# Kernel optimization log

Hardware: AMD Instinct MI355X
Metric: run time of the kernel (lower is better)

Reference implementation:

```python
import jax, jax.numpy as jnp
import numpy as np

B, L, N = 8, 720, 321
D_MODEL, H, E_LAYERS, PRED = 512, 8, 2, 336
D_HEAD = D_MODEL // H
D_FF = 128
FACTOR = 5
U = min(int(FACTOR * np.ceil(np.log(L))), L)  # = 35: top-u queries and sample size
EPS = 1e-5


def _layer_norm(x, g, b):
    mu = x.mean(-1, keepdims=True)
    var = ((x - mu) ** 2).mean(-1, keepdims=True)
    return (x - mu) / jnp.sqrt(var + EPS) * g + b


def _prob_attention(q, k, v, samp_idx):
    # Informer ProbSparse attention (mask_flag=False). q,k,v: [B,H,L,Dh]
    Bq, Hq, Lq, Dh = q.shape
    k_samp = k[:, :, samp_idx, :]                                   # [B,H,L,S,Dh]
    qk_samp = jnp.einsum('bhld,bhlsd->bhls', q, k_samp)             # sampled scores
    M = qk_samp.max(-1) - qk_samp.sum(-1) / Lq                      # sparsity measure
    _, m_top = jax.lax.top_k(M, U)                                  # [B,H,U]
    q_red = jnp.take_along_axis(q, m_top[..., None], axis=2)        # [B,H,U,Dh]
    scores = jnp.einsum('bhud,bhld->bhul', q_red, k) * (1.0 / np.sqrt(Dh))
    attn = jax.nn.softmax(scores, axis=-1)
    upd = jnp.einsum('bhul,bhld->bhud', attn, v)                    # [B,H,U,Dh]
    ctx = jnp.broadcast_to(v.mean(axis=2, keepdims=True), q.shape)  # mean-V init
    b_idx = jnp.arange(Bq)[:, None, None]
    h_idx = jnp.arange(Hq)[None, :, None]
    return ctx.at[b_idx, h_idx, m_top].set(upd)


def _forward(x_enc, embed_w, embed_b, wq, bq, wk, bk, wv, bv, wo, bo,
             ln1_g, ln1_b, w1, b1, w2, b2, ln2_g, ln2_b,
             wout, bout, wg, bg, samp_idx):
    x = jnp.transpose(x_enc, (0, 2, 1))                             # [B,N,L]
    mean = x.mean(-1, keepdims=True)
    std = jnp.std(x, axis=-1, ddof=1, keepdims=True) + EPS
    xs = (x - mean) / std
    h = jnp.transpose(xs, (0, 2, 1)) @ embed_w + embed_b            # [B,L,Dm]
    y = jnp.zeros((B, L, PRED), dtype=h.dtype)

    def heads(t):
        return jnp.transpose(t.reshape(B, L, H, D_HEAD), (0, 2, 1, 3))

    for l in range(E_LAYERS):
        q = heads(h @ wq[l] + bq[l])
        k = heads(h @ wk[l] + bk[l])
        v = heads(h @ wv[l] + bv[l])
        ctx = _prob_attention(q, k, v, samp_idx)
        ctx = jnp.transpose(ctx, (0, 2, 1, 3)).reshape(B, L, D_MODEL)
        attn_out = ctx @ wo[l] + bo[l]
        hx = _layer_norm(h - attn_out, ln1_g[l], ln1_b[l])          # Minusformer subtraction
        ff = jax.nn.relu(hx @ w1[l] + b1[l]) @ w2[l] + b2[l]
        h = _layer_norm(hx - ff, ln2_g[l], ln2_b[l])
        y = y + (h @ wout[l] + bout[l]) * jax.nn.sigmoid(h @ wg[l] + bg[l])
    out = y[:, :N, :] * std + mean                                  # inverse scaling [B,N,PRED]
    return jnp.transpose(out, (0, 2, 1))                            # [B,PRED,N]


def setup_inputs() -> dict:
    key = jax.random.key(0)
    ks = jax.random.split(key, 12)
    s = 0.02

    def w(k, shape):
        return jax.random.normal(k, shape, dtype=jnp.float32) * s

    return {
        'x_enc': jax.random.normal(ks[0], (B, L, N), dtype=jnp.float32),
        'samp_idx': jax.random.randint(ks[1], (L, U), 0, L),
        'embed_w': w(ks[2], (N, D_MODEL)),
        'embed_b': jnp.zeros((D_MODEL,), jnp.float32),
        'wq': w(ks[3], (E_LAYERS, D_MODEL, D_MODEL)),
        'bq': jnp.zeros((E_LAYERS, D_MODEL), jnp.float32),
        'wk': w(ks[4], (E_LAYERS, D_MODEL, D_MODEL)),
        'bk': jnp.zeros((E_LAYERS, D_MODEL), jnp.float32),
        'wv': w(ks[5], (E_LAYERS, D_MODEL, D_MODEL)),
        'bv': jnp.zeros((E_LAYERS, D_MODEL), jnp.float32),
        'wo': w(ks[6], (E_LAYERS, D_MODEL, D_MODEL)),
        'bo': jnp.zeros((E_LAYERS, D_MODEL), jnp.float32),
        'ln1_g': jnp.ones((E_LAYERS, D_MODEL), jnp.float32),
        'ln1_b': jnp.zeros((E_LAYERS, D_MODEL), jnp.float32),
        'w1': w(ks[7], (E_LAYERS, D_MODEL, D_FF)),
        'b1': jnp.zeros((E_LAYERS, D_FF), jnp.float32),
        'w2': w(ks[8], (E_LAYERS, D_FF, D_MODEL)),
        'b2': jnp.zeros((E_LAYERS, D_MODEL), jnp.float32),
        'ln2_g': jnp.ones((E_LAYERS, D_MODEL), jnp.float32),
        'ln2_b': jnp.zeros((E_LAYERS, D_MODEL), jnp.float32),
        'wout': w(ks[9], (E_LAYERS, D_MODEL, PRED)),
        'bout': jnp.zeros((E_LAYERS, PRED), jnp.float32),
        'wg': w(ks[10], (E_LAYERS, D_MODEL, PRED)),
        'bg': jnp.zeros((E_LAYERS, PRED), jnp.float32),
    }


def reference(x_enc, samp_idx, embed_w, embed_b, wq, bq, wk, bk, wv, bv, wo, bo,
              ln1_g, ln1_b, w1, b1, w2, b2, ln2_g, ln2_b, wout, bout, wg, bg):
    return _forward(x_enc, embed_w, embed_b, wq, bq, wk, bk, wv, bv, wo, bo,
                    ln1_g, ln1_b, w1, b1, w2, b2, ln2_g, ln2_b,
                    wout, bout, wg, bg, samp_idx)
```

## Files before the change

kernel.cpp:

```cpp
#include <hip/hip_runtime.h>
#include <math.h>

#define BB_ 8
#define LL_ 720
#define NF 321
#define DM 512
#define HH_ 8
#define DH 64
#define DFF 128
#define PRED 336
#define UK 35
#define NLAY 2
#define EPSF 1e-5f
#define BL (BB_*LL_)
#define TJC 72
#define NCH (LL_/TJC)
#define LCH 48
#define NLC (LL_/LCH)

typedef unsigned short ushort;
typedef __attribute__((ext_vector_type(4))) float f32x4;
typedef __attribute__((ext_vector_type(8))) ushort ushort8;
typedef __attribute__((ext_vector_type(4))) ushort ushortx4;

#define KVSEG ((size_t)64*LL_*64)

__device__ __forceinline__ float b2f(ushort u){
  unsigned int x = ((unsigned int)u) << 16;
  return __builtin_bit_cast(float, x);
}
__device__ __forceinline__ ushort f2b(float f){
  unsigned int x = __builtin_bit_cast(unsigned int, f);
  unsigned int r = x + 0x7fff + ((x >> 16) & 1);
  return (ushort)(r >> 16);
}

__device__ __forceinline__ float wredsum(float v){
#pragma unroll
  for (int o=32;o>0;o>>=1) v += __shfl_xor(v,o,64);
  return v;
}
__device__ __forceinline__ float wredmax(float v){
#pragma unroll
  for (int o=32;o>0;o>>=1) v = fmaxf(v,__shfl_xor(v,o,64));
  return v;
}
__device__ __forceinline__ float bredsum(float v, float* red){
  int lane = threadIdx.x & 63, wid = threadIdx.x >> 6;
  v = wredsum(v);
  __syncthreads();
  if (lane==0) red[wid]=v;
  __syncthreads();
  return red[0]+red[1]+red[2]+red[3];
}

__global__ __launch_bounds__(256) void stats3_k(const float* __restrict__ x,
                                                float* __restrict__ pp){
  __shared__ float s1[4][64], s2[4][64];
  int blk = blockIdx.x;
  int lc = blk % NLC; int r = blk / NLC;
  int nt = r % 6; int b = r / 6;
  int nl = threadIdx.x & 63, lg = threadIdx.x >> 6;
  int n = nt*64 + nl;
  float sum=0.f, ss=0.f;
  if (n < NF){
    const float* xp = x + ((size_t)b*LL_ + lc*LCH)*NF + n;
    for (int l=lg; l<LCH; l+=4){ float v = xp[(size_t)l*NF]; sum += v; ss = fmaf(v,v,ss); }
  }
  s1[lg][nl]=sum; s2[lg][nl]=ss;
  __syncthreads();
  if (lg==0){
    float S = s1[0][nl]+s1[1][nl]+s1[2][nl]+s1[3][nl];
    float Q = s2[0][nl]+s2[1][nl]+s2[2][nl]+s2[3][nl];
    pp[(size_t)blk*128 + nl]      = S;
    pp[(size_t)blk*128 + 64 + nl] = Q;
  }
}

__global__ __launch_bounds__(64) void statsc_k(const float* __restrict__ pp,
                                               float* __restrict__ mean,
                                               float* __restrict__ stdv,
                                               float* __restrict__ rstd){
  int bn6 = blockIdx.x;
  int nl = threadIdx.x;
  int nt = bn6 % 6, b = bn6 / 6;
  int n = nt*64 + nl;
  if (n >= NF) return;
  float S=0.f, Q=0.f;
#pragma unroll
  for (int lc=0; lc<NLC; ++lc){
    size_t base = ((size_t)(b*6+nt)*NLC + lc)*128;
    S += pp[base + nl];
    Q += pp[base + 64 + nl];
  }
  float mu = S*(1.f/LL_);
  float var = fmaxf((Q - S*mu)*(1.f/(LL_-1)), 0.f);
  float sd = sqrtf(var) + EPSF;
  int bn = b*NF+n;
  mean[bn]=mu; stdv[bn]=sd; rstd[bn]=1.f/sd;
}

#define KPE 352
__global__ __launch_bounds__(256) void xnorm_k(const float* __restrict__ x,
                                               const float* __restrict__ mean,
                                               const float* __restrict__ rstd,
                                               ushort* __restrict__ xn){
  int idx = blockIdx.x*256 + threadIdx.x;
  if (idx >= BL*KPE) return;
  int c = idx % KPE; int bl = idx / KPE; int b = bl / LL_;
  float v = 0.f;
  if (c < NF) v = (x[(size_t)bl*NF + c] - mean[b*NF+c]) * rstd[b*NF+c];
  xn[idx] = f2b(v);
}

struct TDesc { const float* in; ushort* out; int N, K, Npad, Kpad, nbx, blk0, ilv; };
struct TPack { TDesc d[17]; int n; };
__global__ __launch_bounds__(256) void transpose_k(TPack p){
  __shared__ float tile[32][33];
  int blk = blockIdx.x;
  int di = 0;
  while (di+1 < p.n && p.d[di+1].blk0 <= blk) ++di;
  TDesc D = p.d[di];
  int rel = blk - D.blk0;
  int bx = rel % D.nbx, by = rel / D.nbx;
  int k0 = bx*32, n0 = by*32;
  int t = threadIdx.x; int tx = t & 31, ty = t >> 5;
#pragma unroll
  for (int i=0;i<4;++i){
    int k = k0+ty+8*i, n = n0+tx;
    float v = (k < D.K && n < D.N) ? D.in[(size_t)k*D.N + n] : 0.f;
    tile[ty+8*i][tx] = v;
  }
  __syncthreads();
#pragma unroll
  for (int i=0;i<4;++i){
    int n = n0+ty+8*i, k = k0+tx;
    if (n < D.Npad && k < D.Kpad){
      int outn = D.ilv ? (2*n + (D.ilv-1)) : n;
      D.out[(size_t)outn*D.Kpad + k] = f2b(tile[tx][ty+8*i]);
    }
  }
}

__global__ __launch_bounds__(256) void pack_bias_k(const float* __restrict__ bq,
                                                   const float* __restrict__ bk,
                                                   const float* __restrict__ bv,
                                                   const float* __restrict__ bo2,
                                                   const float* __restrict__ bg,
                                                   float* __restrict__ bqkv,
                                                   float* __restrict__ bog){
  int t = blockIdx.x*256 + threadIdx.x;
  if (t < 2*1536){
    int l = t/1536, c = t%1536;
    float v = c<512 ? bq[l*512+c] : (c<1024 ? bk[l*512+c-512] : bv[l*512+c-1024]);
    bqkv[t] = v;
  }
  if (t < 2*672){
    int l = t/672, c = t%672;
    int p = c>>1;
    bog[t] = (c&1) ? bg[l*336+p] : bo2[l*336+p];
  }
}

__global__ __launch_bounds__(256) void gemm_k(
    const ushort* __restrict__ A, const ushort* __restrict__ Bt,
    const float* __restrict__ bias, void* __restrict__ Cout,
    ushort* __restrict__ Cbf, ushort* __restrict__ kvp,
    int N, int K, int flags)
{
  __shared__ ushort As[128*32];
  __shared__ ushort Bs[128*32];
  const int t = threadIdx.x;
  const int bm = blockIdx.y << 7, bn = blockIdx.x << 7;
  const int lane = t & 63, wid = t >> 6;
  const int wm = (wid >> 1) << 6, wn = (wid & 1) << 6;
  const int fr = lane & 15, kg = lane >> 4;

  f32x4 acc[4][4];
#pragma unroll
  for (int i=0;i<4;++i)
#pragma unroll
    for (int j=0;j<4;++j) acc[i][j] = (f32x4){0.f,0.f,0.f,0.f};

  const int rA0 = t >> 2,        qA0 = t & 3;
  const int rA1 = (t+256) >> 2;
  const size_t aOff0 = (size_t)(bm + rA0)*K + qA0*8;
  const size_t aOff1 = (size_t)(bm + rA1)*K + qA0*8;
  const size_t bOff0 = (size_t)(bn + rA0)*K + qA0*8;
  const size_t bOff1 = (size_t)(bn + rA1)*K + qA0*8;
  const int lA0 = (rA0<<5) + ((qA0 ^ ((rA0>>1)&3))<<3);
  const int lA1 = (rA1<<5) + ((qA0 ^ ((rA1>>1)&3))<<3);

  for (int k0=0; k0<K; k0+=32){
    ushort8 va0 = *(const ushort8*)(A  + aOff0 + k0);
    ushort8 va1 = *(const ushort8*)(A  + aOff1 + k0);
    ushort8 vb0 = *(const ushort8*)(Bt + bOff0 + k0);
    ushort8 vb1 = *(const ushort8*)(Bt + bOff1 + k0);
    *(ushort8*)&As[lA0] = va0;
    *(ushort8*)&As[lA1] = va1;
    *(ushort8*)&Bs[lA0] = vb0;
    *(ushort8*)&Bs[lA1] = vb1;
    __syncthreads();
    ushort8 af[4], bfr[4];
#pragma unroll
    for (int i=0;i<4;++i){
      int ra = wm + (i<<4) + fr;
      af[i]  = *(const ushort8*)&As[(ra<<5) + ((kg ^ ((ra>>1)&3))<<3)];
      int rb = wn + (i<<4) + fr;
      bfr[i] = *(const ushort8*)&Bs[(rb<<5) + ((kg ^ ((rb>>1)&3))<<3)];
    }
#pragma unroll
    for (int i=0;i<4;++i)
#pragma unroll
      for (int j=0;j<4;++j)
        asm("v_mfma_f32_16x16x32_bf16 %0, %1, %2, %0"
            : "+v"(acc[i][j]) : "v"(af[i]), "v"(bfr[j]));
    __syncthreads();
  }

  const int colBase = bn + wn + fr;
  const int rowBase = bm + wm + (kg << 2);

  if (flags & 16){
#pragma unroll
    for (int j=0;j<4;++j){
      int col = colBase + (j<<4);
      if (col >= N) continue;
      float bv = bias[col];
#pragma unroll
      for (int i=0;i<4;++i){
        int row0 = rowBase + (i<<4);
#pragma unroll
        for (int r=0;r<4;++r){
          float v = acc[i][j][r] + bv;
          float o = __shfl_xor(v, 1, 64);
          if ((lane & 1) == 0){
            float val = v * (1.f/(1.f+__expf(-o)));
            size_t yi = (size_t)(row0+r)*PRED + (col>>1);
            float* yp = (float*)Cout;
            yp[yi] = (flags & 32) ? (yp[yi] + val) : val;
          }
        }
      }
    }
    return;
  }

#pragma unroll
  for (int j=0;j<4;++j){
    int col = colBase + (j<<4);
    if (col >= N) continue;
    float bv = bias[col];
#pragma unroll
    for (int i=0;i<4;++i){
      int row0 = rowBase + (i<<4);
#pragma unroll
      for (int r=0;r<4;++r){
        float v = acc[i][j][r] + bv;
        if (flags & 1) v = fmaxf(v, 0.f);
        int row = row0 + r;
        size_t idx = (size_t)row*N + col;
        if (flags & 2) ((ushort*)Cout)[idx] = f2b(v);
        else if (flags & 8){
          if (col < 512) ((float*)Cout)[idx] = v;
          else {
            int hh = (col >> 6) & 7;
            int dd = col & 63;
            int bb = row / LL_; int jr = row - bb*LL_;
            ushort bfv = f2b(v);
            if (col < 1024){
              kvp[((size_t)(bb*8+hh)*64 + dd)*LL_ + jr] = bfv;
              kvp[2*KVSEG + ((size_t)(bb*8+hh)*LL_ + jr)*64 + dd] = bfv;
            } else {
              kvp[KVSEG + ((size_t)(bb*8+hh)*LL_ + jr)*64 + dd] = bfv;
            }
          }
        } else {
          ((float*)Cout)[idx] = v;
          if (flags & 4) Cbf[idx] = f2b(v);
        }
      }
    }
  }
}

__global__ __launch_bounds__(256) void msc_k(const float* __restrict__ qkv,
                                             const ushort* __restrict__ kR,
                                             const int* __restrict__ samp,
                                             float* __restrict__ Mb){
  __shared__ float sq[4][64];
  int wid = threadIdx.x >> 6, lane = threadIdx.x & 63;
  int gid = blockIdx.x*4 + wid;
  int l = gid % LL_; int bh = gid / LL_; int h = bh & 7; int b = bh >> 3;
  sq[wid][lane] = qkv[(size_t)(b*LL_ + l)*1536 + h*64 + lane];
  __syncthreads();
  float acc = 0.f;
  if (lane < UK){
    int j = samp[l*UK + lane];
    const ushort8* kr = (const ushort8*)(kR + ((size_t)bh*LL_ + j)*64);
    const float* sqw = sq[wid];
#pragma unroll
    for (int d8=0; d8<8; ++d8){
      ushort8 kk = kr[d8];
#pragma unroll
      for (int e=0;e<8;++e) acc = fmaf(sqw[d8*8+e], b2f(kk[e]), acc);
    }
  }
  float mx = (lane < UK) ? acc : -INFINITY;
  float sm = (lane < UK) ? acc : 0.f;
  mx = wredmax(mx);
  sm = wredsum(sm);
  if (lane == 0) Mb[gid] = mx - sm*(1.f/LL_);
}

__global__ __launch_bounds__(64) void topk2_k(const float* __restrict__ Mb,
                                              int* __restrict__ mtop){
  int bh = blockIdx.x; int lane = threadIdx.x;
  const float* mp = Mb + (size_t)bh*LL_;
  float v[12]; int vi[12];
#pragma unroll
  for (int i=0;i<12;++i){
    int j = lane + i*64;
    bool ok = j < LL_;
    v[i] = ok ? mp[j] : -INFINITY;
    vi[i] = ok ? j : (LL_ + i);
  }
  for (int it=0; it<UK; ++it){
    float best = v[0]; int bi = vi[0]; int bslot = 0;
#pragma unroll
    for (int i=1;i<12;++i){
      if (v[i] > best || (v[i]==best && vi[i] < bi)){ best=v[i]; bi=vi[i]; bslot=i; }
    }
    float gb = best; int gi = bi;
#pragma unroll
    for (int o=32;o>0;o>>=1){
      float ov = __shfl_xor(gb,o,64); int oi = __shfl_xor(gi,o,64);
      if (ov > gb || (ov==gb && oi < gi)){ gb=ov; gi=oi; }
    }
    if (lane==0) mtop[(size_t)bh*UK + it] = gi;
    if (bi == gi){
#pragma unroll
      for (int i=0;i<12;++i) if (i==bslot) v[i] = -INFINITY;
    }
  }
}

__global__ __launch_bounds__(256) void vmean_k(const ushort* __restrict__ vp,
                                               float* __restrict__ vmn){
  __shared__ float part[4][64];
  int bh = blockIdx.x;
  int t = threadIdx.x; int d = t & 63, jg = t >> 6;
  const ushort* vb = vp + (size_t)bh*LL_*64 + d;
  float s = 0.f;
  for (int j=jg; j<LL_; j+=4) s += b2f(vb[(size_t)j*64]);
  part[jg][d] = s;
  __syncthreads();
  if (t < 64) vmn[bh*64+t] = (part[0][t]+part[1][t]+part[2][t]+part[3][t])*(1.f/LL_);
}

__global__ __launch_bounds__(256) void ctxfill_k(const float* __restrict__ vmn,
                                                 ushort* __restrict__ ctx){
  int idx = blockIdx.x*256 + threadIdx.x;
  int c4 = idx & 127; int bl = idx >> 7; int b = bl / LL_;
  int c = c4*4;
  const float* vm = vmn + (b*8 + (c>>6))*64 + (c&63);
  ushortx4 o = { f2b(vm[0]), f2b(vm[1]), f2b(vm[2]), f2b(vm[3]) };
  *(ushortx4*)&ctx[(size_t)bl*DM + c] = o;
}

__global__ __launch_bounds__(256) void attn4_k(const float* __restrict__ qkv,
                                               const ushort* __restrict__ kT,
                                               const ushort* __restrict__ vp,
                                               const int* __restrict__ mtop,
                                               float* __restrict__ pacc,
                                               float* __restrict__ pm,
                                               float* __restrict__ pl){
  __shared__ ushort skT[64][TJC];
  __shared__ ushort sv[TJC][64];
  __shared__ float  sq[UK][64];
  __shared__ float  sc[UK][TJC];
  int blk = blockIdx.x;
  int ch = blk % NCH; int bh = blk / NCH;
  int b = bh >> 3, h = bh & 7; int t0 = ch*TJC;
  int t = threadIdx.x, lane = t & 63, wid = t >> 6;
  for (int idx=t; idx<64*(TJC/8); idx+=256){
    int d = idx/(TJC/8), c8 = idx%(TJC/8);
    *(ushort8*)&skT[d][c8*8] =
      *(const ushort8*)(kT + ((size_t)bh*64 + d)*LL_ + t0 + c8*8);
  }
  for (int idx=t; idx<TJC*8; idx+=256){
    int jj = idx>>3, c8 = idx&7;
    *(ushort8*)&sv[jj][c8*8] =
      *(const ushort8*)(vp + ((size_t)bh*LL_ + t0+jj)*64 + c8*8);
  }
  for (int idx=t; idx<UK*64; idx+=256){
    int u = idx>>6, d = idx&63;
    int row = mtop[bh*UK + u];
    sq[u][d] = qkv[(size_t)(b*LL_ + row)*1536 + h*64 + d];
  }
  __syncthreads();
  for (int idx=t; idx<UK*(TJC/8); idx+=256){
    int u = idx/(TJC/8), jb = idx%(TJC/8);
    float dot[8] = {0.f,0.f,0.f,0.f,0.f,0.f,0.f,0.f};
    const float* qu = sq[u];
#pragma unroll
    for (int d=0; d<64; ++d){
      ushort8 kk = *(const ushort8*)&skT[d][jb*8];
      float qv = qu[d];
#pragma unroll
      for (int e=0;e<8;++e) dot[e] = fmaf(qv, b2f(kk[e]), dot[e]);
    }
#pragma unroll
    for (int e=0;e<8;++e) sc[u][jb*8+e] = dot[e]*0.125f;
  }
  __syncthreads();
  for (int u=wid; u<UK; u+=4){
    float v0 = sc[u][lane];
    float v1 = (lane < TJC-64) ? sc[u][64+lane] : -3.0e38f;
    float mx = wredmax(fmaxf(v0,v1));
    float e0 = __expf(v0-mx);
    float e1 = (lane < TJC-64) ? __expf(v1-mx) : 0.f;
    sc[u][lane] = e0;
    if (lane < TJC-64) sc[u][64+lane] = e1;
    float s = wredsum(e0+e1);
    if (lane==0){
      pm[((size_t)bh*NCH+ch)*UK + u] = mx;
      pl[((size_t)bh*NCH+ch)*UK + u] = s;
    }
  }
  __syncthreads();
  for (int idx=t; idx<UK*64; idx+=256){
    int u = idx>>6, d = idx&63;
    const float* scu = sc[u];
    float a = 0.f;
#pragma unroll 8
    for (int jj=0; jj<TJC; ++jj) a = fmaf(scu[jj], b2f(sv[jj][d]), a);
    pacc[(((size_t)bh*NCH+ch)*UK + u)*64 + d] = a;
  }
}

__global__ __launch_bounds__(256) void attn5_k(const float* __restrict__ pacc,
                                               const float* __restrict__ pm,
                                               const float* __restrict__ pl,
                                               const int* __restrict__ mtop,
                                               ushort* __restrict__ ctx){
  int bh = blockIdx.x; int b = bh >> 3, h = bh & 7;
  int t = threadIdx.x;
  for (int idx=t; idx<UK*64; idx+=256){
    int u = idx>>6, d = idx&63;
    float M = -3.0e38f;
#pragma unroll
    for (int ch=0; ch<NCH; ++ch)
      M = fmaxf(M, pm[((size_t)bh*NCH+ch)*UK + u]);
    float L = 0.f, A = 0.f;
#pragma unroll
    for (int ch=0; ch<NCH; ++ch){
      float w = __expf(pm[((size_t)bh*NCH+ch)*UK + u] - M);
      L += w * pl[((size_t)bh*NCH+ch)*UK + u];
      A += w * pacc[(((size_t)bh*NCH+ch)*UK + u)*64 + d];
    }
    int row = mtop[bh*UK + u];
    ctx[(size_t)(b*LL_ + row)*DM + h*64 + d] = f2b(A / L);
  }
}

__global__ __launch_bounds__(256) void subln_k(const float* __restrict__ a,
                                               const float* __restrict__ s,
                                               const float* __restrict__ g,
                                               const float* __restrict__ be,
                                               float* __restrict__ of32,
                                               ushort* __restrict__ obf){
  __shared__ float red[4];
  int row = blockIdx.x;
  size_t base = (size_t)row * DM;
  int t = threadIdx.x;
  float e0 = a[base+t]     - s[base+t];
  float e1 = a[base+t+256] - s[base+t+256];
  float sum = bredsum(e0+e1, red);
  float mu = sum * (1.f/DM);
  float d0 = e0-mu, d1 = e1-mu;
  __syncthreads();
  float var = bredsum(d0*d0+d1*d1, red);
  float rs = rsqrtf(var*(1.f/DM) + EPSF);
  float o0 = d0*rs*g[t]     + be[t];
  float o1 = d1*rs*g[t+256] + be[t+256];
  of32[base+t]     = o0;
  of32[base+t+256] = o1;
  obf[base+t]      = f2b(o0);
  obf[base+t+256]  = f2b(o1);
}

__global__ __launch_bounds__(256) void final2_k(const float* __restrict__ y,
                                                const float* __restrict__ stdv,
                                                const float* __restrict__ mean,
                                                float* __restrict__ out){
  __shared__ float tile[32][33];
  int n0 = blockIdx.x*32, p0 = blockIdx.y*32, b = blockIdx.z;
  int tx = threadIdx.x & 31, ty = threadIdx.x >> 5;
  for (int i=ty; i<32; i+=8){
    int n = n0+i, p = p0+tx;
    tile[i][tx] = (n<NF && p<PRED) ? y[((size_t)b*LL_+n)*PRED + p] : 0.f;
  }
  __syncthreads();
  for (int i=ty; i<32; i+=8){
    int p = p0+i, n = n0+tx;
    if (p<PRED && n<NF)
      out[((size_t)b*PRED + p)*NF + n] = tile[tx][i]*stdv[b*NF+n] + mean[b*NF+n];
  }
}

extern "C" void kernel_launch(void* const* d_in, const int* in_sizes, int n_in,
                              void* d_out, int out_size, void* d_ws, size_t ws_size,
                              hipStream_t stream){
  const float* x_enc = (const float*)d_in[0];
  const int*   samp  = (const int*)  d_in[1];
  const float* embw  = (const float*)d_in[2];
  const float* embb  = (const float*)d_in[3];
  const float* wq    = (const float*)d_in[4];
  const float* bq    = (const float*)d_in[5];
  const float* wk    = (const float*)d_in[6];
  const float* bk    = (const float*)d_in[7];
  const float* wv    = (const float*)d_in[8];
  const float* bv    = (const float*)d_in[9];
  const float* wo    = (const float*)d_in[10];
  const float* bo    = (const float*)d_in[11];
  const float* ln1g  = (const float*)d_in[12];
  const float* ln1b  = (const float*)d_in[13];
  const float* w1    = (const float*)d_in[14];
  const float* b1    = (const float*)d_in[15];
  const float* w2    = (const float*)d_in[16];
  const float* b2    = (const float*)d_in[17];
  const float* ln2g  = (const float*)d_in[18];
  const float* ln2b  = (const float*)d_in[19];
  const float* wout  = (const float*)d_in[20];
  const float* boutp = (const float*)d_in[21];
  const float* wg    = (const float*)d_in[22];
  const float* bg    = (const float*)d_in[23];
  float* out = (float*)d_out;

  char* wsb = (char*)d_ws;
  size_t off = 0;
  auto alloc = [&](size_t bytes)->void*{
    void* p = wsb + off; off += (bytes + 255) & ~(size_t)255; return p;
  };
  float* mean  = (float*)alloc((size_t)BB_*NF*4);
  float* stdv  = (float*)alloc((size_t)BB_*NF*4);
  float* rstd  = (float*)alloc((size_t)BB_*NF*4);
  float* pp    = (float*)alloc((size_t)BB_*6*NLC*128*4);
  float* bqkv  = (float*)alloc(2*1536*4);
  float* bog   = (float*)alloc(2*672*4);
  ushort* xn     = (ushort*)alloc((size_t)BL*KPE*2);
  ushort* we_t   = (ushort*)alloc((size_t)512*KPE*2);
  ushort* wqkv_t = (ushort*)alloc((size_t)2*1536*512*2);
  ushort* wo_t   = (ushort*)alloc((size_t)2*512*512*2);
  ushort* w1_t   = (ushort*)alloc((size_t)2*128*512*2);
  ushort* w2_t   = (ushort*)alloc((size_t)2*512*128*2);
  ushort* wog_t  = (ushort*)alloc((size_t)2*768*512*2);
  ushort* h_bf   = (ushort*)alloc((size_t)BL*DM*2);
  ushort* hx_bf  = (ushort*)alloc((size_t)BL*DM*2);
  ushort* ctx_bf = (ushort*)alloc((size_t)BL*DM*2);
  ushort* ff1_bf = (ushort*)alloc((size_t)BL*DFF*2);
  ushort* kvpack = (ushort*)alloc(3*KVSEG*2);
  float* h_f32   = (float*)alloc((size_t)BL*DM*4);
  float* hx_f32  = (float*)alloc((size_t)BL*DM*4);
  float* qkv = (float*)alloc((size_t)BL*1536*4);
  float* tmp = (float*)alloc((size_t)BL*DM*4);
  float* y   = (float*)alloc((size_t)BL*PRED*4);
  float* Mb  = (float*)alloc((size_t)BB_*HH_*LL_*4);
  int*  mtop = (int*)  alloc((size_t)BB_*HH_*UK*4);
  float* vmn = (float*)alloc((size_t)BB_*HH_*DH*4);
  float* pacc = (float*)alloc((size_t)64*NCH*UK*64*4);
  float* pm   = (float*)alloc((size_t)64*NCH*UK*4);
  float* pl   = (float*)alloc((size_t)64*NCH*UK*4);
  if (off > ws_size) return;
  ushort* kTp   = kvpack;
  ushort* vpack = kvpack + KVSEG;
  ushort* kRp   = kvpack + 2*KVSEG;

  stats3_k<<<BB_*6*NLC, 256, 0, stream>>>(x_enc, pp);
  statsc_k<<<BB_*6, 64, 0, stream>>>(pp, mean, stdv, rstd);
  xnorm_k<<<(BL*KPE+255)/256, 256, 0, stream>>>(x_enc, mean, rstd, xn);

  TPack tp; int blk = 0; int di = 0;
  auto addT = [&](const float* in, ushort* o, int N, int K, int Npad, int Kpad, int ilv){
    TDesc& d = tp.d[di++]; d.in=in; d.out=o; d.N=N; d.K=K; d.Npad=Npad; d.Kpad=Kpad; d.ilv=ilv;
    d.nbx = (Kpad+31)/32; d.blk0 = blk; blk += d.nbx * ((Npad+31)/32);
  };
  addT(embw, we_t, 512, NF, 512, KPE, 0);
  for (int l=0;l<NLAY;++l){
    addT(wq + (size_t)l*262144, wqkv_t + (size_t)l*786432,            512,512,512,512,0);
    addT(wk + (size_t)l*262144, wqkv_t + (size_t)l*786432 + 262144,   512,512,512,512,0);
    addT(wv + (size_t)l*262144, wqkv_t + (size_t)l*786432 + 524288,   512,512,512,512,0);
    addT(wo + (size_t)l*262144, wo_t   + (size_t)l*262144,            512,512,512,512,0);
    addT(w1 + (size_t)l*65536,  w1_t   + (size_t)l*65536,             128,512,128,512,0);
    addT(w2 + (size_t)l*65536,  w2_t   + (size_t)l*65536,             512,128,512,128,0);
    addT(wout + (size_t)l*172032, wog_t + (size_t)l*393216,           336,512,384,512,1);
    addT(wg   + (size_t)l*172032, wog_t + (size_t)l*393216,           336,512,384,512,2);
  }
  tp.n = di;
  transpose_k<<<blk, 256, 0, stream>>>(tp);
  pack_bias_k<<<12, 256, 0, stream>>>(bq, bk, bv, boutp, bg, bqkv, bog);

  gemm_k<<<dim3(4,45), 256, 0, stream>>>(xn, we_t, embb, h_f32, h_bf, nullptr,
                                         512, KPE, 4);

  for (int l=0;l<NLAY;++l){
    gemm_k<<<dim3(12,45), 256, 0, stream>>>(h_bf, wqkv_t + (size_t)l*786432,
                                            bqkv + l*1536, qkv, nullptr, kvpack,
                                            1536, 512, 8);
    msc_k<<<BB_*HH_*LL_/4, 256, 0, stream>>>(qkv, kRp, samp, Mb);
    topk2_k<<<BB_*HH_, 64, 0, stream>>>(Mb, mtop);
    vmean_k<<<BB_*HH_, 256, 0, stream>>>(vpack, vmn);
    ctxfill_k<<<BL*DM/1024, 256, 0, stream>>>(vmn, ctx_bf);
    attn4_k<<<64*NCH, 256, 0, stream>>>(qkv, kTp, vpack, mtop, pacc, pm, pl);
    attn5_k<<<64, 256, 0, stream>>>(pacc, pm, pl, mtop, ctx_bf);
    gemm_k<<<dim3(4,45), 256, 0, stream>>>(ctx_bf, wo_t + (size_t)l*262144,
                                           bo + l*512, tmp, nullptr, nullptr,
                                           512, 512, 0);
    subln_k<<<BL, 256, 0, stream>>>(h_f32, tmp, ln1g + l*512, ln1b + l*512,
                                    hx_f32, hx_bf);
    gemm_k<<<dim3(1,45), 256, 0, stream>>>(hx_bf, w1_t + (size_t)l*65536,
                                           b1 + l*128, ff1_bf, nullptr, nullptr,
                                           128, 512, 3);
    gemm_k<<<dim3(4,45), 256, 0, stream>>>(ff1_bf, w2_t + (size_t)l*65536,
                                           b2 + l*512, tmp, nullptr, nullptr,
                                           512, 128, 0);
    subln_k<<<BL, 256, 0, stream>>>(hx_f32, tmp, ln2g + l*512, ln2b + l*512,
                                    h_f32, h_bf);
    gemm_k<<<dim3(6,45), 256, 0, stream>>>(h_bf, wog_t + (size_t)l*393216,
                                           bog + l*672, y, nullptr, nullptr,
                                           672, 512, 16 | (l ? 32 : 0));
  }
  final2_k<<<dim3((NF+31)/32,(PRED+31)/32,BB_), 256, 0, stream>>>(y, stdv, mean, out);
}
```

Measured before the change: 717.9 us.

## Drop transposed K copy and fold V-mean into attention kernel

The QKV GEMM epilogue no longer writes a separate transposed K buffer. attn4_k now loads row-major K and transposes it into shared memory itself. The V mean is also computed inside attn4_k as per-chunk partial sums from the already-staged V tile, then reduced by a tiny vmnc_k kernel, which replaces the separate vmean_k pass over V. This cuts global scatter writes and one full read of V, at the cost of strided shared-memory transposes that may cause bank conflicts.

```diff
diff --git a/kernel.cpp b/kernel.cpp
--- a/kernel.cpp
+++ b/kernel.cpp
@@ -268,12 +268,10 @@
             int dd = col & 63;
             int bb = row / LL_; int jr = row - bb*LL_;
             ushort bfv = f2b(v);
-            if (col < 1024){
-              kvp[((size_t)(bb*8+hh)*64 + dd)*LL_ + jr] = bfv;
-              kvp[2*KVSEG + ((size_t)(bb*8+hh)*LL_ + jr)*64 + dd] = bfv;
-            } else {
+            if (col < 1024)
+              kvp[((size_t)(bb*8+hh)*LL_ + jr)*64 + dd] = bfv;
+            else
               kvp[KVSEG + ((size_t)(bb*8+hh)*LL_ + jr)*64 + dd] = bfv;
-            }
           }
         } else {
           ((float*)Cout)[idx] = v;
@@ -345,17 +343,15 @@
   }
 }
 
-__global__ __launch_bounds__(256) void vmean_k(const ushort* __restrict__ vp,
-                                               float* __restrict__ vmn){
-  __shared__ float part[4][64];
-  int bh = blockIdx.x;
-  int t = threadIdx.x; int d = t & 63, jg = t >> 6;
-  const ushort* vb = vp + (size_t)bh*LL_*64 + d;
+__global__ __launch_bounds__(256) void vmnc_k(const float* __restrict__ pvs,
+                                              float* __restrict__ vmn){
+  int idx = blockIdx.x*256 + threadIdx.x;
+  if (idx >= 64*64) return;
+  int bh = idx >> 6, d = idx & 63;
   float s = 0.f;
-  for (int j=jg; j<LL_; j+=4) s += b2f(vb[(size_t)j*64]);
-  part[jg][d] = s;
-  __syncthreads();
-  if (t < 64) vmn[bh*64+t] = (part[0][t]+part[1][t]+part[2][t]+part[3][t])*(1.f/LL_);
+#pragma unroll
+  for (int ch=0; ch<NCH; ++ch) s += pvs[((size_t)bh*NCH + ch)*64 + d];
+  vmn[idx] = s*(1.f/LL_);
 }
 
 __global__ __launch_bounds__(256) void ctxfill_k(const float* __restrict__ vmn,
@@ -369,24 +365,27 @@
 }
 
 __global__ __launch_bounds__(256) void attn4_k(const float* __restrict__ qkv,
-                                               const ushort* __restrict__ kT,
+                                               const ushort* __restrict__ kR,
                                                const ushort* __restrict__ vp,
                                                const int* __restrict__ mtop,
                                                float* __restrict__ pacc,
                                                float* __restrict__ pm,
-                                               float* __restrict__ pl){
+                                               float* __restrict__ pl,
+                                               float* __restrict__ pvs){
   __shared__ ushort skT[64][TJC];
   __shared__ ushort sv[TJC][64];
   __shared__ float  sq[UK][64];
   __shared__ float  sc[UK][TJC];
+  __shared__ float  part[4][64];
   int blk = blockIdx.x;
   int ch = blk % NCH; int bh = blk / NCH;
   int b = bh >> 3, h = bh & 7; int t0 = ch*TJC;
   int t = threadIdx.x, lane = t & 63, wid = t >> 6;
-  for (int idx=t; idx<64*(TJC/8); idx+=256){
-    int d = idx/(TJC/8), c8 = idx%(TJC/8);
-    *(ushort8*)&skT[d][c8*8] =
-      *(const ushort8*)(kT + ((size_t)bh*64 + d)*LL_ + t0 + c8*8);
+  for (int idx=t; idx<TJC*8; idx+=256){
+    int jj = idx>>3, c8 = idx&7;
+    ushort8 kk = *(const ushort8*)(kR + ((size_t)bh*LL_ + t0+jj)*64 + c8*8);
+#pragma unroll
+    for (int e=0;e<8;++e) skT[c8*8+e][jj] = kk[e];
   }
   for (int idx=t; idx<TJC*8; idx+=256){
     int jj = idx>>3, c8 = idx&7;
@@ -399,6 +398,12 @@
     sq[u][d] = qkv[(size_t)(b*LL_ + row)*1536 + h*64 + d];
   }
   __syncthreads();
+  {
+    int d = t & 63, q = t >> 6;
+    float s = 0.f;
+    for (int jj=q; jj<TJC; jj+=4) s += b2f(sv[jj][d]);
+    part[q][d] = s;
+  }
   for (int idx=t; idx<UK*(TJC/8); idx+=256){
     int u = idx/(TJC/8), jb = idx%(TJC/8);
     float dot[8] = {0.f,0.f,0.f,0.f,0.f,0.f,0.f,0.f};
@@ -414,6 +419,8 @@
     for (int e=0;e<8;++e) sc[u][jb*8+e] = dot[e]*0.125f;
   }
   __syncthreads();
+  if (t < 64)
+    pvs[((size_t)bh*NCH + ch)*64 + t] = part[0][t]+part[1][t]+part[2][t]+part[3][t];
   for (int u=wid; u<UK; u+=4){
     float v0 = sc[u][lane];
     float v1 = (lane < TJC-64) ? sc[u][64+lane] : -3.0e38f;
@@ -560,7 +567,7 @@
   ushort* hx_bf  = (ushort*)alloc((size_t)BL*DM*2);
   ushort* ctx_bf = (ushort*)alloc((size_t)BL*DM*2);
   ushort* ff1_bf = (ushort*)alloc((size_t)BL*DFF*2);
-  ushort* kvpack = (ushort*)alloc(3*KVSEG*2);
+  ushort* kvpack = (ushort*)alloc(2*KVSEG*2);
   float* h_f32   = (float*)alloc((size_t)BL*DM*4);
   float* hx_f32  = (float*)alloc((size_t)BL*DM*4);
   float* qkv = (float*)alloc((size_t)BL*1536*4);
@@ -572,10 +579,10 @@
   float* pacc = (float*)alloc((size_t)64*NCH*UK*64*4);
   float* pm   = (float*)alloc((size_t)64*NCH*UK*4);
   float* pl   = (float*)alloc((size_t)64*NCH*UK*4);
+  float* pvs  = (float*)alloc((size_t)64*NCH*64*4);
   if (off > ws_size) return;
-  ushort* kTp   = kvpack;
+  ushort* kRp   = kvpack;
   ushort* vpack = kvpack + KVSEG;
-  ushort* kRp   = kvpack + 2*KVSEG;
 
   stats3_k<<<BB_*6*NLC, 256, 0, stream>>>(x_enc, pp);
   statsc_k<<<BB_*6, 64, 0, stream>>>(pp, mean, stdv, rstd);
@@ -610,9 +617,9 @@
                                             1536, 512, 8);
     msc_k<<<BB_*HH_*LL_/4, 256, 0, stream>>>(qkv, kRp, samp, Mb);
     topk2_k<<<BB_*HH_, 64, 0, stream>>>(Mb, mtop);
-    vmean_k<<<BB_*HH_, 256, 0, stream>>>(vpack, vmn);
+    attn4_k<<<64*NCH, 256, 0, stream>>>(qkv, kRp, vpack, mtop, pacc, pm, pl, pvs);
+    vmnc_k<<<16, 256, 0, stream>>>(pvs, vmn);
     ctxfill_k<<<BL*DM/1024, 256, 0, stream>>>(vmn, ctx_bf);
-    attn4_k<<<64*NCH, 256, 0, stream>>>(qkv, kTp, vpack, mtop, pacc, pm, pl);
     attn5_k<<<64, 256, 0, stream>>>(pacc, pm, pl, mtop, ctx_bf);
     gemm_k<<<dim3(4,45), 256, 0, stream>>>(ctx_bf, wo_t + (size_t)l*262144,
                                            bo + l*512, tmp, nullptr, nullptr,
```

New measurement: 623.3 us. 13.2% less time.
